# Performance work log

Hardware: AMD Instinct MI355X
Metric: run time of the kernel (lower is better)

The kernel has to match this reference:

```python
import jax, jax.numpy as jnp
import numpy as np
from jax import lax

HEADS = 4
SR = 4
LN_EPS = 1e-5


def setup_inputs() -> dict:
    key = jax.random.key(0)
    ks = jax.random.split(key, 8)
    B, N, C = 8, 4096, 256
    w_scale = 0.05  # keep attention logits in a sane range
    return {
        "x": jax.random.normal(ks[0], (B, N, C), jnp.float32),
        "h": 64,
        "w": 64,
        "Wq": jax.random.normal(ks[1], (C, C), jnp.float32) * w_scale,
        "Wkv": jax.random.normal(ks[2], (C, 2 * C), jnp.float32) * w_scale,
        "sr_w": jax.random.normal(ks[3], (C, C, SR, SR), jnp.float32) * w_scale,
        "sr_b": jnp.zeros((C,), jnp.float32),
        "ln_g": jnp.ones((C,), jnp.float32),
        "ln_b": jnp.zeros((C,), jnp.float32),
        "Wo": jax.random.normal(ks[4], (C, C), jnp.float32) * w_scale,
        "bo": jnp.zeros((C,), jnp.float32),
    }


def _layernorm(x, g, b):
    mu = x.mean(-1, keepdims=True)
    var = ((x - mu) ** 2).mean(-1, keepdims=True)
    return (x - mu) * lax.rsqrt(var + LN_EPS) * g + b


def reference(x, h, w, Wq, Wkv, sr_w, sr_b, ln_g, ln_b, Wo, bo):
    B, N, C = x.shape
    hd = C // HEADS
    scale = hd ** -0.5
    # Q projection -> [B, H, N, hd]
    q = (x @ Wq).reshape(B, N, HEADS, hd).transpose(0, 2, 1, 3)
    # spatial reduction of K/V tokens: strided conv + LayerNorm
    x_kv = x.transpose(0, 2, 1).reshape(B, C, h, w)  # b (h w) c -> b c h w
    x_kv = lax.conv_general_dilated(
        x_kv, sr_w, window_strides=(SR, SR), padding="VALID",
        dimension_numbers=("NCHW", "OIHW", "NCHW"))
    x_kv = x_kv + sr_b[None, :, None, None]
    Nk = (h // SR) * (w // SR)
    x_kv = x_kv.reshape(B, C, Nk).transpose(0, 2, 1)  # b c h w -> b (h w) c
    x_kv = _layernorm(x_kv, ln_g, ln_b)
    # KV projection -> k, v each [B, H, Nk, hd]
    kv = (x_kv @ Wkv).reshape(B, Nk, 2, HEADS, hd)
    k = kv[:, :, 0].transpose(0, 2, 1, 3)
    v = kv[:, :, 1].transpose(0, 2, 1, 3)
    # attention: full [B, H, N, Nk] score matrix, softmax over kv axis
    att = jax.nn.softmax(jnp.einsum("bhxd,bhyd->bhxy", q, k) * scale, axis=-1)
    out = jnp.einsum("bhxy,bhyd->bhxd", att, v)
    out = out.transpose(0, 2, 1, 3).reshape(B, N, C)  # b h l d -> b l (h d)
    return out @ Wo + bo
```

## Files before the change

kernel.cpp:

```cpp
#include <hip/hip_runtime.h>

typedef __bf16 bf16;
typedef bf16 bf16x8 __attribute__((ext_vector_type(8)));
typedef bf16 bf16x4 __attribute__((ext_vector_type(4)));
typedef float f32x4 __attribute__((ext_vector_type(4)));

#define MFMA16(a, b, c) __builtin_amdgcn_mfma_f32_16x16x32_bf16(a, b, c, 0, 0, 0)

__device__ __forceinline__ void gload_lds16(const bf16* g, bf16* l) {
  __builtin_amdgcn_global_load_lds(
      (const __attribute__((address_space(1))) void*)g,
      (__attribute__((address_space(3))) void*)l, 16, 0, 0);
}

__global__ void k_prep(const float* __restrict__ x, const float* __restrict__ Wq,
                       const float* __restrict__ Wkv, const float* __restrict__ Wo,
                       const float* __restrict__ srw,
                       bf16* __restrict__ x_bf, bf16* __restrict__ WqT,
                       bf16* __restrict__ WkvT, bf16* __restrict__ WoT,
                       bf16* __restrict__ srwT) {
  int bid = blockIdx.x, tid = threadIdx.x;
  if (bid < 8192) {
    int i = (bid * 256 + tid) * 4;
    float4 v = *(const float4*)(x + i);
    bf16x4 o;
    o[0] = (bf16)v.x; o[1] = (bf16)v.y; o[2] = (bf16)v.z; o[3] = (bf16)v.w;
    *(bf16x4*)(x_bf + i) = o;
  } else if (bid < 9216) {
    int id = (bid - 8192) * 256 + tid;
    if (id < 65536) {
      int c = id >> 8, r = id & 255;
      WqT[id] = (bf16)Wq[r * 256 + c];
    } else if (id < 196608) {
      int l = id - 65536;
      int c = l >> 8, r = l & 255;
      WkvT[l] = (bf16)Wkv[r * 512 + c];
    } else {
      int l = id - 196608;
      int c = l >> 8, r = l & 255;
      WoT[l] = (bf16)Wo[r * 256 + c];
    }
  } else {
    int id4 = ((bid - 9216) * 256 + tid) * 4;
    int o = id4 >> 12, rem = id4 & 4095;
    int i = rem >> 4, p = rem & 15;
    float4 v = *(const float4*)(srw + id4);
    srwT[(o << 12) + ((p + 0) << 8) + i] = (bf16)v.x;
    srwT[(o << 12) + ((p + 1) << 8) + i] = (bf16)v.y;
    srwT[(o << 12) + ((p + 2) << 8) + i] = (bf16)v.z;
    srwT[(o << 12) + ((p + 3) << 8) + i] = (bf16)v.w;
  }
}

template <int AMODE, int EMODE>
__global__ __launch_bounds__(256, 2) void k_gemm(
    const bf16* __restrict__ A, const bf16* __restrict__ Bt,
    void* __restrict__ Cout, const float* __restrict__ bias,
    int M, int N, int K) {
  constexpr int LDT = 72;
  __shared__ alignas(16) bf16 As[64 * LDT];
  __shared__ alignas(16) bf16 Bs[64 * LDT];
  int tid = threadIdx.x;
  int m0 = blockIdx.x * 64, n0 = blockIdx.y * 64;
  int kbeg = blockIdx.z * K;
  int wave = tid >> 6, lane = tid & 63;
  int quad = lane >> 4, l16 = lane & 15;

  f32x4 acc[4];
#pragma unroll
  for (int i = 0; i < 4; i++) acc[i] = (f32x4){0.f, 0.f, 0.f, 0.f};

  for (int k0 = kbeg; k0 < kbeg + K; k0 += 64) {
#pragma unroll
    for (int t = 0; t < 2; t++) {
      int c = tid + t * 256;
      int row = c >> 3, c8 = (c & 7) * 8;
      const bf16* asrc;
      if constexpr (AMODE == 0) {
        asrc = A + (size_t)(m0 + row) * K + k0 + c8;
      } else {
        int m = m0 + row;
        int b = m >> 8, tt = m & 255;
        int oh = tt >> 4, ow = tt & 15;
        int p = k0 >> 8;
        int kh = p >> 2, kw = p & 3;
        int tok = (oh * 4 + kh) * 64 + ow * 4 + kw;
        asrc = A + ((size_t)(b * 4096 + tok) << 8) + (k0 & 255) + c8;
      }
      *(bf16x8*)&As[row * LDT + c8] = *(const bf16x8*)asrc;
      *(bf16x8*)&Bs[row * LDT + c8] =
          *(const bf16x8*)(Bt + (size_t)(n0 + row) * ((AMODE == 1) ? 4096 : K) + k0 + c8);
    }
    __syncthreads();
#pragma unroll
    for (int kk = 0; kk < 64; kk += 32) {
      bf16x8 af = *(const bf16x8*)&As[(wave * 16 + l16) * LDT + kk + quad * 8];
#pragma unroll
      for (int nt = 0; nt < 4; nt++) {
        bf16x8 bfr = *(const bf16x8*)&Bs[(nt * 16 + l16) * LDT + kk + quad * 8];
        acc[nt] = MFMA16(af, bfr, acc[nt]);
      }
    }
    __syncthreads();
  }

  int rbase = m0 + wave * 16 + quad * 4;
#pragma unroll
  for (int nt = 0; nt < 4; nt++) {
    int col = n0 + nt * 16 + l16;
#pragma unroll
    for (int r = 0; r < 4; r++) {
      float v = acc[nt][r];
      int row = rbase + r;
      if constexpr (EMODE == 2) {
        int b = row >> 8, key = row & 255;
        int isv = col >> 8, c2 = col & 255;
        int hh = c2 >> 6, d = c2 & 63;
        int bh = b * 4 + hh;
        bf16* dst = (bf16*)Cout;
        if (isv == 0)
          dst[(((size_t)bh) * 256 + key) * 64 + (d ^ ((key & 7) << 3))] = (bf16)v;
        else
          dst[32 * 256 * 64 + (((size_t)bh) * 64 + d) * 256 + (key ^ ((d & 7) << 3))] = (bf16)v;
      } else if constexpr (EMODE == 3) {
        ((float*)Cout)[(size_t)row * N + col] = v + bias[col];
      } else if constexpr (EMODE == 5) {
        int b2 = row >> 12, tok = row & 4095;
        int hh = col >> 6, d = col & 63;
        ((bf16*)Cout)[(((size_t)(b2 * 4 + hh)) * 4096 + tok) * 64 + d] = (bf16)v;
      } else {
        ((float*)Cout)[((size_t)blockIdx.z * M + row) * N + col] = v;
      }
    }
  }
}

__global__ void k_ln(const float* __restrict__ part, const float* __restrict__ srb,
                     const float* __restrict__ g, const float* __restrict__ bb,
                     bf16* __restrict__ out) {
  int row = blockIdx.x * 4 + (threadIdx.x >> 6);
  int lane = threadIdx.x & 63;
  size_t off = (size_t)row * 256 + lane * 4;
  float4 v = *(const float4*)&part[off];
#pragma unroll
  for (int z = 1; z < 8; z++) {
    float4 p = *(const float4*)&part[(size_t)z * 2048 * 256 + off];
    v.x += p.x; v.y += p.y; v.z += p.z; v.w += p.w;
  }
  int c = lane * 4;
  v.x += srb[c + 0]; v.y += srb[c + 1]; v.z += srb[c + 2]; v.w += srb[c + 3];
  float s = v.x + v.y + v.z + v.w;
#pragma unroll
  for (int i = 1; i < 64; i <<= 1) s += __shfl_xor(s, i, 64);
  float mu = s * (1.f / 256.f);
  float d0 = v.x - mu, d1 = v.y - mu, d2 = v.z - mu, d3 = v.w - mu;
  float q = d0 * d0 + d1 * d1 + d2 * d2 + d3 * d3;
#pragma unroll
  for (int i = 1; i < 64; i <<= 1) q += __shfl_xor(q, i, 64);
  float rs = rsqrtf(q * (1.f / 256.f) + 1e-5f);
  bf16x4 o;
  o[0] = (bf16)(d0 * rs * g[c + 0] + bb[c + 0]);
  o[1] = (bf16)(d1 * rs * g[c + 1] + bb[c + 1]);
  o[2] = (bf16)(d2 * rs * g[c + 2] + bb[c + 2]);
  o[3] = (bf16)(d3 * rs * g[c + 3] + bb[c + 3]);
  *(bf16x4*)&out[(size_t)row * 256 + c] = o;
}

__global__ __launch_bounds__(256, 3) void k_attn(
    const bf16* __restrict__ Qg,
    const bf16* __restrict__ Kg,
    const bf16* __restrict__ Vg,
    bf16* __restrict__ O) {
  int bh = blockIdx.x, qt = blockIdx.y;
  int b = bh >> 2, h = bh & 3;
  int tid = threadIdx.x, wave = tid >> 6, lane = tid & 63;
  int quad = lane >> 4, l16 = lane & 15;

  __shared__ alignas(16) bf16 smem[24576];
  bf16* Ks = smem;
  bf16* Vs = smem + 16384;

  const bf16* Kbh = Kg + ((size_t)bh << 14);
  const bf16* Vbh = Vg + ((size_t)bh << 14);

#pragma unroll
  for (int t = 0; t < 8; t++) {
    int chunk = t * 4 + wave;
    gload_lds16(Kbh + chunk * 512 + lane * 8, Ks + chunk * 512);
  }
#pragma unroll
  for (int t = 0; t < 4; t++) {
    int chunk = t * 4 + wave;
    gload_lds16(Vbh + (chunk * 4 + (lane >> 4)) * 256 + (lane & 15) * 8,
                Vs + chunk * 512);
  }

  const bf16* qrow =
      Qg + (((size_t)bh * 4096) + qt * 64 + wave * 16 + l16) * 64 + quad * 8;
  bf16x8 aq0 = *(const bf16x8*)(qrow);
  bf16x8 aq1 = *(const bf16x8*)(qrow + 32);

  __syncthreads();

  f32x4 s[16];
#pragma unroll
  for (int i = 0; i < 16; i++) s[i] = (f32x4){0.f, 0.f, 0.f, 0.f};
#pragma unroll
  for (int nt = 0; nt < 16; nt++) {
    int krow = nt * 16 + l16;
    const bf16* kb = Ks + krow * 64;
    int sw = (krow & 7) << 3;
    bf16x8 b0 = *(const bf16x8*)(kb + ((quad * 8) ^ sw));
    bf16x8 b1 = *(const bf16x8*)(kb + ((32 + quad * 8) ^ sw));
    s[nt] = MFMA16(aq0, b0, s[nt]);
    s[nt] = MFMA16(aq1, b1, s[nt]);
  }

  const float scale = 0.125f;
#pragma unroll
  for (int r = 0; r < 4; r++) {
    float m = -1e30f;
#pragma unroll
    for (int nt = 0; nt < 16; nt++) m = fmaxf(m, s[nt][r]);
#pragma unroll
    for (int i = 1; i < 16; i <<= 1) m = fmaxf(m, __shfl_xor(m, i, 64));
    float sum = 0.f;
#pragma unroll
    for (int nt = 0; nt < 16; nt++) {
      float e = __expf((s[nt][r] - m) * scale);
      s[nt][r] = e;
      sum += e;
    }
#pragma unroll
    for (int i = 1; i < 16; i <<= 1) sum += __shfl_xor(sum, i, 64);
    float inv = 1.f / sum;
#pragma unroll
    for (int nt = 0; nt < 16; nt++) s[nt][r] *= inv;
  }

  __syncthreads();

#pragma unroll
  for (int nt = 0; nt < 16; nt++)
#pragma unroll
    for (int r = 0; r < 4; r++) {
      int prow = wave * 16 + quad * 4 + r;
      Ks[prow * 256 + ((nt * 16 + l16) ^ ((prow & 7) << 3))] = (bf16)s[nt][r];
    }

  int arow = wave * 16 + l16;
  int asw = (arow & 7) << 3;
  const bf16* pb = Ks + arow * 256;
  f32x4 o[4];
#pragma unroll
  for (int i = 0; i < 4; i++) o[i] = (f32x4){0.f, 0.f, 0.f, 0.f};
#pragma unroll
  for (int k0 = 0; k0 < 128; k0 += 32) {
    bf16x8 ap = *(const bf16x8*)(pb + ((k0 + quad * 8) ^ asw));
#pragma unroll
    for (int nt = 0; nt < 4; nt++) {
      int vrow = nt * 16 + l16;
      bf16x8 bv = *(const bf16x8*)(Vs + vrow * 128 + ((k0 + quad * 8) ^ ((vrow & 7) << 3)));
      o[nt] = MFMA16(ap, bv, o[nt]);
    }
  }

  __syncthreads();
#pragma unroll
  for (int t = 0; t < 4; t++) {
    int chunk = t * 4 + wave;
    gload_lds16(Vbh + (chunk * 4 + (lane >> 4)) * 256 + 128 + (lane & 15) * 8,
                Vs + chunk * 512);
  }
  __syncthreads();

#pragma unroll
  for (int k0 = 128; k0 < 256; k0 += 32) {
    bf16x8 ap = *(const bf16x8*)(pb + ((k0 + quad * 8) ^ asw));
    int kl = k0 - 128;
#pragma unroll
    for (int nt = 0; nt < 4; nt++) {
      int vrow = nt * 16 + l16;
      bf16x8 bv = *(const bf16x8*)(Vs + vrow * 128 + ((kl + quad * 8) ^ ((vrow & 7) << 3)));
      o[nt] = MFMA16(ap, bv, o[nt]);
    }
  }

  size_t orow = (size_t)b * 4096 + qt * 64 + wave * 16 + quad * 4;
#pragma unroll
  for (int nt = 0; nt < 4; nt++) {
    int col = h * 64 + nt * 16 + l16;
#pragma unroll
    for (int r = 0; r < 4; r++) O[(orow + r) * 256 + col] = (bf16)o[nt][r];
  }
}

extern "C" void kernel_launch(void* const* d_in, const int* in_sizes, int n_in,
                              void* d_out, int out_size, void* d_ws, size_t ws_size,
                              hipStream_t stream) {
  (void)in_sizes; (void)n_in; (void)out_size; (void)ws_size;
  const float* x   = (const float*)d_in[0];
  const float* Wq  = (const float*)d_in[3];
  const float* Wkv = (const float*)d_in[4];
  const float* srw = (const float*)d_in[5];
  const float* srb = (const float*)d_in[6];
  const float* lng = (const float*)d_in[7];
  const float* lnb = (const float*)d_in[8];
  const float* Wo  = (const float*)d_in[9];
  const float* bo  = (const float*)d_in[10];
  float* out = (float*)d_out;

  char* ws = (char*)d_ws;
  bf16*  x_bf  = (bf16*)(ws + 0);
  bf16*  AObuf = (bf16*)(ws + 16777216);
  float* convp = (float*)(ws + 33554432);
  bf16*  qbuf  = (bf16*)(ws + 33554432);
  bf16*  WqT   = (bf16*)(ws + 50331648);
  bf16*  WkvT  = (bf16*)(ws + 50462720);
  bf16*  WoT   = (bf16*)(ws + 50724864);
  bf16*  srwT  = (bf16*)(ws + 50855936);
  bf16*  xln   = (bf16*)(ws + 52953088);
  bf16*  kvbuf = (bf16*)(ws + 54001664);

  k_prep<<<10240, 256, 0, stream>>>(x, Wq, Wkv, Wo, srw, x_bf, WqT, WkvT, WoT, srwT);
  k_gemm<1, 4><<<dim3(32, 4, 8), 256, 0, stream>>>(x_bf, srwT, convp, nullptr, 2048, 256, 512);
  k_ln<<<512, 256, 0, stream>>>(convp, srb, lng, lnb, xln);
  k_gemm<0, 2><<<dim3(32, 8), 256, 0, stream>>>(xln, WkvT, kvbuf, nullptr, 2048, 512, 256);
  k_gemm<0, 5><<<dim3(512, 4), 256, 0, stream>>>(x_bf, WqT, qbuf, nullptr, 32768, 256, 256);
  k_attn<<<dim3(32, 64), 256, 0, stream>>>(qbuf, kvbuf, kvbuf + (size_t)32 * 256 * 64, AObuf);
  k_gemm<0, 3><<<dim3(512, 4), 256, 0, stream>>>(AObuf, WoT, out, bo, 32768, 256, 256);
}
```

Before: 187.8 us.

## Add 128x128 GEMM kernel with direct-to-LDS loads for conv, Q and output projections

Introduces a new GEMM kernel that computes a 128x128 tile per block, with each of four waves owning a 64x64 sub-tile. Tiles are loaded straight into LDS using global_load_lds. It replaces the 64x64 kernel for the strided-conv GEMM, the Q projection and the output projection, which should raise arithmetic intensity and cut load instructions. The old kernel is trimmed to the KV-projection path only. The trade-offs are an unpadded LDS layout that can cause bank conflicts on fragment reads, higher register pressure, and fewer blocks for the small conv GEMM.

```diff
diff --git a/kernel.cpp b/kernel.cpp
--- a/kernel.cpp
+++ b/kernel.cpp
@@ -75,21 +75,10 @@
     for (int t = 0; t < 2; t++) {
       int c = tid + t * 256;
       int row = c >> 3, c8 = (c & 7) * 8;
-      const bf16* asrc;
-      if constexpr (AMODE == 0) {
-        asrc = A + (size_t)(m0 + row) * K + k0 + c8;
-      } else {
-        int m = m0 + row;
-        int b = m >> 8, tt = m & 255;
-        int oh = tt >> 4, ow = tt & 15;
-        int p = k0 >> 8;
-        int kh = p >> 2, kw = p & 3;
-        int tok = (oh * 4 + kh) * 64 + ow * 4 + kw;
-        asrc = A + ((size_t)(b * 4096 + tok) << 8) + (k0 & 255) + c8;
-      }
-      *(bf16x8*)&As[row * LDT + c8] = *(const bf16x8*)asrc;
+      *(bf16x8*)&As[row * LDT + c8] =
+          *(const bf16x8*)(A + (size_t)(m0 + row) * K + k0 + c8);
       *(bf16x8*)&Bs[row * LDT + c8] =
-          *(const bf16x8*)(Bt + (size_t)(n0 + row) * ((AMODE == 1) ? 4096 : K) + k0 + c8);
+          *(const bf16x8*)(Bt + (size_t)(n0 + row) * K + k0 + c8);
     }
     __syncthreads();
 #pragma unroll
@@ -122,14 +111,93 @@
           dst[(((size_t)bh) * 256 + key) * 64 + (d ^ ((key & 7) << 3))] = (bf16)v;
         else
           dst[32 * 256 * 64 + (((size_t)bh) * 64 + d) * 256 + (key ^ ((d & 7) << 3))] = (bf16)v;
-      } else if constexpr (EMODE == 3) {
+      } else {
         ((float*)Cout)[(size_t)row * N + col] = v + bias[col];
-      } else if constexpr (EMODE == 5) {
-        int b2 = row >> 12, tok = row & 4095;
-        int hh = col >> 6, d = col & 63;
-        ((bf16*)Cout)[(((size_t)(b2 * 4 + hh)) * 4096 + tok) * 64 + d] = (bf16)v;
+      }
+    }
+  }
+}
+
+template <int AMODE, int EMODE>
+__global__ __launch_bounds__(256, 2) void k_gemm128(
+    const bf16* __restrict__ A, const bf16* __restrict__ Bt,
+    void* __restrict__ Cout, const float* __restrict__ bias,
+    int M, int N, int K) {
+  __shared__ alignas(16) bf16 As[128 * 64];
+  __shared__ alignas(16) bf16 Bs[128 * 64];
+  int tid = threadIdx.x;
+  int m0 = blockIdx.x * 128, n0 = blockIdx.y * 128;
+  int kbeg = blockIdx.z * K;
+  int wave = tid >> 6, lane = tid & 63;
+  int quad = lane >> 4, l16 = lane & 15;
+  int wr = wave >> 1, wc = wave & 1;
+
+  f32x4 acc[4][4];
+#pragma unroll
+  for (int i = 0; i < 4; i++)
+#pragma unroll
+    for (int j = 0; j < 4; j++) acc[i][j] = (f32x4){0.f, 0.f, 0.f, 0.f};
+
+  for (int k0 = kbeg; k0 < kbeg + K; k0 += 64) {
+#pragma unroll
+    for (int t = 0; t < 4; t++) {
+      int chunk = wave * 4 + t;
+      int row = chunk * 8 + (lane >> 3);
+      int c8 = (lane & 7) * 8;
+      const bf16* asrc;
+      if constexpr (AMODE == 0) {
+        asrc = A + (size_t)(m0 + row) * K + k0 + c8;
       } else {
-        ((float*)Cout)[((size_t)blockIdx.z * M + row) * N + col] = v;
+        int m = m0 + row;
+        int b = m >> 8, tt = m & 255;
+        int oh = tt >> 4, ow = tt & 15;
+        int p = k0 >> 8;
+        int kh = p >> 2, kw = p & 3;
+        int tok = (oh * 4 + kh) * 64 + ow * 4 + kw;
+        asrc = A + ((size_t)(b * 4096 + tok) << 8) + (k0 & 255) + c8;
+      }
+      gload_lds16(asrc, As + chunk * 512);
+      gload_lds16(Bt + (size_t)(n0 + row) * ((AMODE == 1) ? 4096 : K) + k0 + c8,
+                  Bs + chunk * 512);
+    }
+    __syncthreads();
+#pragma unroll
+    for (int kk = 0; kk < 64; kk += 32) {
+      bf16x8 af[4], bfr[4];
+#pragma unroll
+      for (int mt = 0; mt < 4; mt++)
+        af[mt] = *(const bf16x8*)&As[(wr * 64 + mt * 16 + l16) * 64 + kk + quad * 8];
+#pragma unroll
+      for (int nt = 0; nt < 4; nt++)
+        bfr[nt] = *(const bf16x8*)&Bs[(wc * 64 + nt * 16 + l16) * 64 + kk + quad * 8];
+#pragma unroll
+      for (int mt = 0; mt < 4; mt++)
+#pragma unroll
+        for (int nt = 0; nt < 4; nt++)
+          acc[mt][nt] = MFMA16(af[mt], bfr[nt], acc[mt][nt]);
+    }
+    __syncthreads();
+  }
+
+#pragma unroll
+  for (int mt = 0; mt < 4; mt++) {
+    int rbase = m0 + wr * 64 + mt * 16 + quad * 4;
+#pragma unroll
+    for (int nt = 0; nt < 4; nt++) {
+      int col = n0 + wc * 64 + nt * 16 + l16;
+#pragma unroll
+      for (int r = 0; r < 4; r++) {
+        float v = acc[mt][nt][r];
+        int row = rbase + r;
+        if constexpr (EMODE == 3) {
+          ((float*)Cout)[(size_t)row * N + col] = v + bias[col];
+        } else if constexpr (EMODE == 5) {
+          int b2 = row >> 12, tok = row & 4095;
+          int hh = col >> 6, d = col & 63;
+          ((bf16*)Cout)[(((size_t)(b2 * 4 + hh)) * 4096 + tok) * 64 + d] = (bf16)v;
+        } else {
+          ((float*)Cout)[((size_t)blockIdx.z * M + row) * N + col] = v;
+        }
       }
     }
   }
@@ -323,10 +391,10 @@
   bf16*  kvbuf = (bf16*)(ws + 54001664);
 
   k_prep<<<10240, 256, 0, stream>>>(x, Wq, Wkv, Wo, srw, x_bf, WqT, WkvT, WoT, srwT);
-  k_gemm<1, 4><<<dim3(32, 4, 8), 256, 0, stream>>>(x_bf, srwT, convp, nullptr, 2048, 256, 512);
+  k_gemm128<1, 4><<<dim3(16, 2, 8), 256, 0, stream>>>(x_bf, srwT, convp, nullptr, 2048, 256, 512);
   k_ln<<<512, 256, 0, stream>>>(convp, srb, lng, lnb, xln);
   k_gemm<0, 2><<<dim3(32, 8), 256, 0, stream>>>(xln, WkvT, kvbuf, nullptr, 2048, 512, 256);
-  k_gemm<0, 5><<<dim3(512, 4), 256, 0, stream>>>(x_bf, WqT, qbuf, nullptr, 32768, 256, 256);
+  k_gemm128<0, 5><<<dim3(256, 2), 256, 0, stream>>>(x_bf, WqT, qbuf, nullptr, 32768, 256, 256);
   k_attn<<<dim3(32, 64), 256, 0, stream>>>(qbuf, kvbuf, kvbuf + (size_t)32 * 256 * 64, AObuf);
-  k_gemm<0, 3><<<dim3(512, 4), 256, 0, stream>>>(AObuf, WoT, out, bo, 32768, 256, 256);
-}
+  k_gemm128<0, 3><<<dim3(256, 2), 256, 0, stream>>>(AObuf, WoT, out, bo, 32768, 256, 256);
+}
```

After: 181.7 us. -3.3%, faster.
